# Kernel tuning notes

Hardware: AMD Instinct MI355X
Metric: run time of the kernel (lower is better)

Reference implementation:

```python
import jax, jax.numpy as jnp
import numpy as np

N_NODES = 100000
N_EDGES = 1600000
IN_DIM = 128
OUT_DIM = 64
HEADS = 4
NEG_SLOPE = 0.2  # PyG GATConv default
LN_EPS = 1e-5


def setup_inputs() -> dict:
    key = jax.random.key(0)
    ks = jax.random.split(key, 8)
    x = jax.random.normal(ks[0], (N_NODES, IN_DIM), dtype=jnp.float32)
    edge_index = jax.random.randint(ks[1], (2, N_EDGES), 0, N_NODES, dtype=jnp.int64)
    # GATConv params: lin weight, per-head attention vectors, output bias (concat=False)
    s = 1.0 / np.sqrt(IN_DIM)
    W = jax.random.uniform(ks[2], (IN_DIM, HEADS * OUT_DIM), jnp.float32, -s, s)
    att_src = jax.random.uniform(ks[3], (HEADS, OUT_DIM), jnp.float32, -s, s)
    att_dst = jax.random.uniform(ks[4], (HEADS, OUT_DIM), jnp.float32, -s, s)
    bias = jnp.zeros((OUT_DIM,), jnp.float32)
    gamma = jnp.ones((OUT_DIM,), jnp.float32)
    beta = jnp.zeros((OUT_DIM,), jnp.float32)
    return {"x": x, "edge_index": edge_index, "W": W, "att_src": att_src,
            "att_dst": att_dst, "bias": bias, "gamma": gamma, "beta": beta}


def reference(x, edge_index, W, att_src, att_dst, bias, gamma, beta):
    N = x.shape[0]
    H, C = att_src.shape
    # Linear projection, split heads: (N, H, C)
    xl = (x @ W).reshape(N, H, C)
    # Per-node attention logits: (N, H)
    a_src = jnp.einsum('nhc,hc->nh', xl, att_src)
    a_dst = jnp.einsum('nhc,hc->nh', xl, att_dst)
    # Add self-loops (PyG GATConv default add_self_loops=True)
    loops = jnp.arange(N, dtype=edge_index.dtype)
    src = jnp.concatenate([edge_index[0], loops])  # (E+N,)
    dst = jnp.concatenate([edge_index[1], loops])
    # Per-edge attention: gather, leaky_relu, segment softmax over destination
    alpha = jax.nn.leaky_relu(a_src[src] + a_dst[dst], NEG_SLOPE)  # (E+N, H)
    amax = jax.ops.segment_max(alpha, dst, num_segments=N)  # (N, H)
    e = jnp.exp(alpha - amax[dst])
    denom = jax.ops.segment_sum(e, dst, num_segments=N)  # (N, H)
    alpha = e / (denom[dst] + 1e-16)
    # Message passing: scatter-add alpha-weighted source features to dst
    msg = xl[src] * alpha[:, :, None]  # (E+N, H, C)
    out = jax.ops.segment_sum(msg, dst, num_segments=N)  # (N, H, C)
    out = out.mean(axis=1) + bias  # concat=False -> head average, (N, C)
    # LayerNorm
    mu = out.mean(axis=-1, keepdims=True)
    var = out.var(axis=-1, keepdims=True)
    return (out - mu) * jax.lax.rsqrt(var + LN_EPS) * gamma + beta
```

## Files before the change

### kernel.cpp

```cpp
#include <hip/hip_runtime.h>
#include <hip/hip_fp16.h>

#define IN_DIM   128
#define HC       256
#define OUT_DIM  64
#define HEADS    4
#define NEG_SLOPE 0.2f
#define LN_EPS   1e-5f
#define MAXBINS  512
#define NHIST    128
#define SCAT_TPE 16

typedef short bf16x8 __attribute__((ext_vector_type(8)));
typedef float f32x4  __attribute__((ext_vector_type(4)));

__device__ __forceinline__ float lrelu(float a){ return a > 0.f ? a : NEG_SLOPE * a; }

__device__ __forceinline__ unsigned short f2bf(float f){
  unsigned u = __float_as_uint(f);
  u = u + 0x7fffu + ((u >> 16) & 1u);
  return (unsigned short)(u >> 16);
}
__device__ __forceinline__ unsigned pk2(float a, float b){
  return (unsigned)f2bf(a) | ((unsigned)f2bf(b) << 16);
}
__device__ __forceinline__ __half2 u2h(unsigned u){ return *(__half2*)&u; }
__device__ __forceinline__ unsigned h2u(__half2 h){ return *(unsigned*)&h; }

__device__ __forceinline__ bool detect32(const int* ei){
  int ln = threadIdx.x & 63;
  unsigned probe = (ln < 32) ? (unsigned)ei[2*ln + 1] : 0u;
  return __ballot(probe != 0) != 0ull;
}

__global__ __launch_bounds__(256) void k_front(
    const float* __restrict__ W, unsigned short* __restrict__ Wt,
    const int* ei, int* __restrict__ partials, int E, int nbins)
{
  if (blockIdx.x < 128){
    int n = blockIdx.x*2 + (threadIdx.x >> 7);
    int k = threadIdx.x & 127;
    Wt[n*IN_DIM + k] = f2bf(W[k*HC + n]);
    return;
  }
  __shared__ int h[MAXBINS];
  bool i32 = detect32(ei);
  for (int i = threadIdx.x; i < nbins; i += 256) h[i] = 0;
  __syncthreads();
  int slot = blockIdx.x - 128;
  if (i32){
    const int* dstp = ei + E;
    for (int e = slot*256 + threadIdx.x; e < E; e += NHIST*256)
      atomicAdd(&h[dstp[e] >> 8], 1);
  } else {
    const long long* dstp = (const long long*)ei + E;
    for (int e = slot*256 + threadIdx.x; e < E; e += NHIST*256)
      atomicAdd(&h[(int)dstp[e] >> 8], 1);
  }
  __syncthreads();
  for (int i = threadIdx.x; i < nbins; i += 256)
    partials[slot*MAXBINS + i] = h[i];
}

__global__ __launch_bounds__(512) void k_binscan(const int* __restrict__ partials,
    int* binstart, int* bincur, int* rowstart, int nbins, int N, int E){
  __shared__ int sh[512];
  int tid = threadIdx.x;
  int v = 0;
  if (tid < nbins)
    for (int j = 0; j < NHIST; ++j) v += partials[j*MAXBINS + tid];
  sh[tid] = v; __syncthreads();
  #pragma unroll
  for (int off = 1; off < 512; off <<= 1){
    int t = (tid >= off) ? sh[tid-off] : 0;
    __syncthreads();
    sh[tid] += t;
    __syncthreads();
  }
  int ex = sh[tid] - v;
  if (tid < nbins){ binstart[tid] = ex; bincur[tid] = ex; }
  if (tid == 0){ binstart[nbins] = E; rowstart[N] = E; }
}

__device__ __forceinline__ void gemm_body(int bid, char* smem,
    const float* __restrict__ x, const unsigned short* __restrict__ Wt,
    const float* __restrict__ att_s, const float* __restrict__ att_d,
    __half* __restrict__ xl_t, float* __restrict__ a_src,
    float* __restrict__ a_dst, int N)
{
  unsigned short* sxl = (unsigned short*)(smem + 16384);
  int t = threadIdx.x;
  int nb = bid * 64;

  #pragma unroll
  for (int it = 0; it < 4; ++it){
    int idx = it*256 + t;
    int row = idx >> 4, seg = idx & 15;
    uint4 pk = make_uint4(0,0,0,0);
    if (nb + row < N){
      const float* xr = x + (size_t)(nb + row)*IN_DIM + seg*8;
      float4 f0 = *(const float4*)xr;
      float4 f1 = *(const float4*)(xr + 4);
      pk.x = pk2(f0.x, f0.y); pk.y = pk2(f0.z, f0.w);
      pk.z = pk2(f1.x, f1.y); pk.w = pk2(f1.z, f1.w);
    }
    int byte = (row*256 + seg*16) ^ ((row & 7) << 4);
    *(uint4*)(smem + byte) = pk;
  }
  __syncthreads();

  int w = t >> 6, l = t & 63;

  bf16x8 bfr[4][4];
  #pragma unroll
  for (int nt = 0; nt < 4; ++nt){
    int col = w*64 + nt*16 + (l & 15);
    #pragma unroll
    for (int ks = 0; ks < 4; ++ks)
      bfr[nt][ks] = *(const bf16x8*)(Wt + (size_t)col*IN_DIM + ks*32 + ((l >> 4) << 3));
  }
  float attS[4], attD[4];
  #pragma unroll
  for (int nt = 0; nt < 4; ++nt){
    attS[nt] = att_s[w*64 + nt*16 + (l & 15)];
    attD[nt] = att_d[w*64 + nt*16 + (l & 15)];
  }

  #pragma unroll
  for (int sub = 0; sub < 4; ++sub){
    bf16x8 afr[4];
    #pragma unroll
    for (int ks = 0; ks < 4; ++ks){
      int row = sub*16 + (l & 15);
      int byte = (row*256 + ks*64 + ((l >> 4) << 4)) ^ ((row & 7) << 4);
      afr[ks] = *(const bf16x8*)(smem + byte);
    }
    f32x4 acc[4] = {{0,0,0,0},{0,0,0,0},{0,0,0,0},{0,0,0,0}};
    #pragma unroll
    for (int nt = 0; nt < 4; ++nt)
      #pragma unroll
      for (int ks = 0; ks < 4; ++ks)
        acc[nt] = __builtin_amdgcn_mfma_f32_16x16x32_bf16(afr[ks], bfr[nt][ks], acc[nt], 0, 0, 0);

    #pragma unroll
    for (int r = 0; r < 4; ++r){
      float ps = 0.f, pd = 0.f;
      #pragma unroll
      for (int nt = 0; nt < 4; ++nt){
        ps = fmaf(acc[nt][r], attS[nt], ps);
        pd = fmaf(acc[nt][r], attD[nt], pd);
      }
      #pragma unroll
      for (int o = 8; o; o >>= 1){ ps += __shfl_xor(ps, o); pd += __shfl_xor(pd, o); }
      int node = nb + sub*16 + (l >> 4)*4 + r;
      if ((l & 15) == 0 && node < N){
        a_src[node*4 + w] = ps;
        a_dst[node*4 + w] = pd;
      }
    }

    #pragma unroll
    for (int nt = 0; nt < 4; ++nt){
      int ch = nt*16 + (l & 15);
      #pragma unroll
      for (int r = 0; r < 4; ++r){
        int row = sub*16 + (l >> 4)*4 + r;
        sxl[row*HC + ch*4 + w] = __half_as_ushort(__float2half(acc[nt][r]));
      }
    }
  }
  __syncthreads();
  const uint4* s4 = (const uint4*)sxl;
  uint4* g4 = (uint4*)(xl_t + (size_t)nb*HC);
  for (int c = t; c < 2048; c += 256){
    int row = c >> 5;
    if (nb + row < N) g4[c] = s4[c];
  }
}

__device__ __forceinline__ void scat_body(int bid, char* smem,
    const int* ei, int* bincur, unsigned* tmp, int E, int nbins)
{
  int* h    = (int*)smem;
  int* base = (int*)(smem + 2048);
  bool i32 = detect32(ei);
  int tile0 = bid * (256*SCAT_TPE);
  for (int i = threadIdx.x; i < nbins; i += 256) h[i] = 0;
  __syncthreads();
  unsigned pk[SCAT_TPE]; int rk[SCAT_TPE];
  #pragma unroll
  for (int k = 0; k < SCAT_TPE; ++k){
    int e = tile0 + k*256 + threadIdx.x;
    if (e < E){
      int s, d;
      if (i32){ s = ei[e]; d = ei[E + e]; }
      else {
        s = (int)((const long long*)ei)[e];
        d = (int)((const long long*)ei)[(size_t)E + e];
      }
      int b = d >> 8;
      pk[k] = (unsigned)s | ((unsigned)(d & 255) << 20);
      rk[k] = atomicAdd(&h[b], 1) | (b << 16);
    }
  }
  __syncthreads();
  for (int i = threadIdx.x; i < nbins; i += 256)
    base[i] = h[i] ? atomicAdd(&bincur[i], h[i]) : 0;
  __syncthreads();
  #pragma unroll
  for (int k = 0; k < SCAT_TPE; ++k){
    int e = tile0 + k*256 + threadIdx.x;
    if (e < E){
      int b = rk[k] >> 16, r = rk[k] & 0xFFFF;
      tmp[base[b] + r] = pk[k];
    }
  }
}

__global__ __launch_bounds__(256) void k_gemm_scat(
    const float* __restrict__ x, const unsigned short* __restrict__ Wt,
    const float* __restrict__ att_s, const float* __restrict__ att_d,
    __half* __restrict__ xl_t, float* __restrict__ a_src, float* __restrict__ a_dst,
    int N, const int* ei, int* bincur, unsigned* tmp, int E, int nbins,
    int gemmBlocks)
{
  __shared__ char smem[49152];
  int bid = (int)blockIdx.x;
  if (bid < gemmBlocks)
    gemm_body(bid, smem, x, Wt, att_s, att_d, xl_t, a_src, a_dst, N);
  else
    scat_body(bid - gemmBlocks, smem, ei, bincur, tmp, E, nbins);
}

__global__ __launch_bounds__(256) void k_binsort(const unsigned* __restrict__ tmp,
    const int* __restrict__ binstart, int* rowstart, int* csr, int N){
  __shared__ int c[256], c2[256], sc[256];
  int b = blockIdx.x, tid = threadIdx.x;
  int s0 = binstart[b], s1 = binstart[b+1];
  c[tid] = 0; c2[tid] = 0;
  __syncthreads();
  for (int e = s0 + tid; e < s1; e += 256)
    atomicAdd(&c[(tmp[e] >> 20) & 255], 1);
  __syncthreads();
  int v = c[tid]; sc[tid] = v;
  __syncthreads();
  #pragma unroll
  for (int off = 1; off < 256; off <<= 1){
    int t = (tid >= off) ? sc[tid-off] : 0;
    __syncthreads();
    sc[tid] += t;
    __syncthreads();
  }
  int ex = sc[tid] - v;
  int d = b*256 + tid;
  if (d < N) rowstart[d] = s0 + ex;
  sc[tid] = ex;
  __syncthreads();
  for (int e = s0 + tid; e < s1; e += 256){
    unsigned u = tmp[e];
    int dl = (u >> 20) & 255;
    int pos = s0 + sc[dl] + atomicAdd(&c2[dl], 1);
    csr[pos] = (int)(u & 0xFFFFFu);
  }
}

__global__ __launch_bounds__(256) void k_node(
    const int* __restrict__ rowstart, const int* __restrict__ csr,
    const float4* __restrict__ a_src4, const float4* __restrict__ a_dst4,
    const __half* __restrict__ xl_t,
    const float* __restrict__ bias, const float* __restrict__ gamma,
    const float* __restrict__ beta, float* __restrict__ out, int N)
{
  __shared__ uint2 wlds[4][4][16];
  __shared__ int   slds[4][4][16];
  int wv = threadIdx.x >> 6, ln = threadIdx.x & 63;
  int g = ln >> 4, i = ln & 15;
  int node = blockIdx.x*16 + wv*4 + g;
  bool alive = node < N;
  int nc = alive ? node : N-1;

  int start = rowstart[nc];
  int end   = alive ? rowstart[nc+1] : start;
  float4 ad  = a_dst4[nc];
  float4 asl = a_src4[nc];

  float es0 = __expf(lrelu(asl.x + ad.x));
  float es1 = __expf(lrelu(asl.y + ad.y));
  float es2 = __expf(lrelu(asl.z + ad.z));
  float es3 = __expf(lrelu(asl.w + ad.w));

  __half2 s01 = __floats2half2_rn(es0, es1);
  __half2 s23 = __floats2half2_rn(es2, es3);
  const uint4* ps = (const uint4*)((const char*)xl_t + ((size_t)nc*512 + (i << 5)));
  uint4 xa = ps[0], xb = ps[1];
  __half2 acc[8];
  acc[0] = __hmul2(s01, u2h(xa.x));
  acc[1] = __hmul2(s23, u2h(xa.y));
  acc[2] = __hmul2(s01, u2h(xa.z));
  acc[3] = __hmul2(s23, u2h(xa.w));
  acc[4] = __hmul2(s01, u2h(xb.x));
  acc[5] = __hmul2(s23, u2h(xb.y));
  acc[6] = __hmul2(s01, u2h(xb.z));
  acc[7] = __hmul2(s23, u2h(xb.w));
  float lp0 = 0.f, lp1 = 0.f, lp2 = 0.f, lp3 = 0.f;

  for (int t = start; ; t += 16){
    int rem = end - t;
    rem = rem < 0 ? 0 : (rem > 16 ? 16 : rem);
    int rmax = rem;
    rmax = max(rmax, __shfl_xor(rmax, 16));
    rmax = max(rmax, __shfl_xor(rmax, 32));
    if (rmax == 0) break;

    int sid = 0;
    float e0 = 0.f, e1 = 0.f, e2 = 0.f, e3 = 0.f;
    if (i < rem){
      sid = csr[t + i];
      float4 as4 = a_src4[sid];
      e0 = __expf(lrelu(as4.x + ad.x));
      e1 = __expf(lrelu(as4.y + ad.y));
      e2 = __expf(lrelu(as4.z + ad.z));
      e3 = __expf(lrelu(as4.w + ad.w));
      lp0 += e0; lp1 += e1; lp2 += e2; lp3 += e3;
    }
    wlds[wv][g][i] = make_uint2(h2u(__floats2half2_rn(e0, e1)),
                                h2u(__floats2half2_rn(e2, e3)));
    slds[wv][g][i] = sid;

    #pragma unroll 2
    for (int j = 0; j < rmax; ++j){
      if (j < rem){
        uint2 wpk = wlds[wv][g][j];
        int sj = slds[wv][g][j];
        __half2 w01 = u2h(wpk.x), w23 = u2h(wpk.y);
        const uint4* p = (const uint4*)((const char*)xl_t + ((size_t)sj*512 + (i << 5)));
        uint4 ya = p[0], yb = p[1];
        acc[0] = __hfma2(w01, u2h(ya.x), acc[0]);
        acc[1] = __hfma2(w23, u2h(ya.y), acc[1]);
        acc[2] = __hfma2(w01, u2h(ya.z), acc[2]);
        acc[3] = __hfma2(w23, u2h(ya.w), acc[3]);
        acc[4] = __hfma2(w01, u2h(yb.x), acc[4]);
        acc[5] = __hfma2(w23, u2h(yb.y), acc[5]);
        acc[6] = __hfma2(w01, u2h(yb.z), acc[6]);
        acc[7] = __hfma2(w23, u2h(yb.w), acc[7]);
      }
    }
  }

  __half2 lp01 = __floats2half2_rn(lp0, lp1);
  __half2 lp23 = __floats2half2_rn(lp2, lp3);
  #pragma unroll
  for (int o = 8; o; o >>= 1){
    lp01 = __hadd2(lp01, u2h(__shfl_xor(h2u(lp01), o)));
    lp23 = __hadd2(lp23, u2h(__shfl_xor(h2u(lp23), o)));
  }
  float r0 = __builtin_amdgcn_rcpf(__low2float(lp01) + es0);
  float r1 = __builtin_amdgcn_rcpf(__high2float(lp01) + es1);
  float r2 = __builtin_amdgcn_rcpf(__low2float(lp23) + es2);
  float r3 = __builtin_amdgcn_rcpf(__high2float(lp23) + es3);

  float4 b4 = *(const float4*)(bias + 4*i);
  float o0 = 0.25f*(__low2float(acc[0])*r0 + __high2float(acc[0])*r1 +
                    __low2float(acc[1])*r2 + __high2float(acc[1])*r3) + b4.x;
  float o1 = 0.25f*(__low2float(acc[2])*r0 + __high2float(acc[2])*r1 +
                    __low2float(acc[3])*r2 + __high2float(acc[3])*r3) + b4.y;
  float o2 = 0.25f*(__low2float(acc[4])*r0 + __high2float(acc[4])*r1 +
                    __low2float(acc[5])*r2 + __high2float(acc[5])*r3) + b4.z;
  float o3 = 0.25f*(__low2float(acc[6])*r0 + __high2float(acc[6])*r1 +
                    __low2float(acc[7])*r2 + __high2float(acc[7])*r3) + b4.w;

  float s  = o0 + o1 + o2 + o3;
  float sq = o0*o0 + o1*o1 + o2*o2 + o3*o3;
  #pragma unroll
  for (int o = 8; o; o >>= 1){
    s  += __shfl_xor(s, o);
    sq += __shfl_xor(sq, o);
  }
  float mu = s * (1.f/OUT_DIM);
  float var = sq * (1.f/OUT_DIM) - mu*mu;
  float rs = rsqrtf(var + LN_EPS);
  float4 g4v = *(const float4*)(gamma + 4*i);
  float4 be4 = *(const float4*)(beta + 4*i);
  if (alive){
    float4 ov;
    ov.x = (o0 - mu)*rs*g4v.x + be4.x;
    ov.y = (o1 - mu)*rs*g4v.y + be4.y;
    ov.z = (o2 - mu)*rs*g4v.z + be4.z;
    ov.w = (o3 - mu)*rs*g4v.w + be4.w;
    *(float4*)(out + (size_t)node*OUT_DIM + 4*i) = ov;
  }
}

extern "C" void kernel_launch(void* const* d_in, const int* in_sizes, int n_in,
                              void* d_out, int out_size, void* d_ws, size_t ws_size,
                              hipStream_t stream)
{
  const float* x     = (const float*)d_in[0];
  const int*   ei    = (const int*)d_in[1];
  const float* W     = (const float*)d_in[2];
  const float* att_s = (const float*)d_in[3];
  const float* att_d = (const float*)d_in[4];
  const float* bias  = (const float*)d_in[5];
  const float* gamma = (const float*)d_in[6];
  const float* beta  = (const float*)d_in[7];
  float* out = (float*)d_out;

  int N = in_sizes[0] / IN_DIM;
  int E = in_sizes[1] / 2;
  int nbins = (N + 255) >> 8;

  char* ws = (char*)d_ws;
  __half* xl_t = (__half*)ws;                   ws += (size_t)N*HC*sizeof(__half);
  float* a_src = (float*)ws;                    ws += (size_t)N*HEADS*sizeof(float);
  float* a_dst = (float*)ws;                    ws += (size_t)N*HEADS*sizeof(float);
  int* rowstart = (int*)ws;                     ws += ((size_t)N+1)*sizeof(int);
  int* csr      = (int*)ws;                     ws += (size_t)E*sizeof(int);
  unsigned* tmp = (unsigned*)ws;                ws += (size_t)E*sizeof(unsigned);
  int* partials = (int*)ws;                     ws += (size_t)NHIST*MAXBINS*sizeof(int);
  int* binstart = (int*)ws;                     ws += (MAXBINS+1)*sizeof(int);
  int* bincur   = (int*)ws;                     ws += MAXBINS*sizeof(int);
  unsigned short* Wt = (unsigned short*)ws;     ws += (size_t)HC*IN_DIM*sizeof(unsigned short);

  int gemmBlocks = (N + 63)/64;
  int scatBlocks = (E + 256*SCAT_TPE - 1)/(256*SCAT_TPE);

  k_front   <<<128 + NHIST, 256, 0, stream>>>(W, Wt, ei, partials, E, nbins);
  k_binscan <<<1, 512, 0, stream>>>(partials, binstart, bincur, rowstart, nbins, N, E);
  k_gemm_scat<<<gemmBlocks + scatBlocks, 256, 0, stream>>>(
      x, Wt, att_s, att_d, xl_t, a_src, a_dst, N, ei, bincur, tmp, E, nbins,
      gemmBlocks);
  k_binsort <<<nbins, 256, 0, stream>>>(tmp, binstart, rowstart, csr, N);
  k_node    <<<(N + 15)/16, 256, 0, stream>>>(rowstart, csr,
              (const float4*)a_src, (const float4*)a_dst, xl_t,
              bias, gamma, beta, out, N);
}
```

Baseline: 221.8 us.

## Fuse per-bin CSR sort into node aggregation kernel with 64-node bins

Shrinks destination bins from 256 to 64 nodes and merges the bin-local counting sort into the aggregation kernel, building each bin's CSR segment in shared memory instead of writing and rereading a global CSR and rowstart. Bin histograms are now combined with global atomics after a memset rather than through a partials array, and the scan is widened to 1024 threads for up to 2048 bins. The GEMM epilogue now streams each 16-row subtile out through a smaller LDS buffer, halving the kernel's static shared memory. In exchange, each node block does more serial work over fewer, larger blocks (one per 64 nodes, 4 nodes per 16-lane group sequentially), which may reduce parallelism and latency hiding in the gather phase.

```diff
diff --git a/kernel.cpp b/kernel.cpp
--- a/kernel.cpp
+++ b/kernel.cpp
@@ -7,8 +7,11 @@
 #define HEADS    4
 #define NEG_SLOPE 0.2f
 #define LN_EPS   1e-5f
-#define MAXBINS  512
-#define NHIST    128
+#define DBITS    6
+#define DPB      64
+#define MAXBINS  2048
+#define CAP      2048
+#define NHIST    256
 #define SCAT_TPE 16
 
 typedef short bf16x8 __attribute__((ext_vector_type(8)));
@@ -35,7 +38,7 @@
 
 __global__ __launch_bounds__(256) void k_front(
     const float* __restrict__ W, unsigned short* __restrict__ Wt,
-    const int* ei, int* __restrict__ partials, int E, int nbins)
+    const int* ei, int* __restrict__ bincnt, int E, int nbins)
 {
   if (blockIdx.x < 128){
     int n = blockIdx.x*2 + (threadIdx.x >> 7);
@@ -51,35 +54,38 @@
   if (i32){
     const int* dstp = ei + E;
     for (int e = slot*256 + threadIdx.x; e < E; e += NHIST*256)
-      atomicAdd(&h[dstp[e] >> 8], 1);
+      atomicAdd(&h[dstp[e] >> DBITS], 1);
   } else {
     const long long* dstp = (const long long*)ei + E;
     for (int e = slot*256 + threadIdx.x; e < E; e += NHIST*256)
-      atomicAdd(&h[(int)dstp[e] >> 8], 1);
+      atomicAdd(&h[((int)dstp[e]) >> DBITS], 1);
   }
   __syncthreads();
   for (int i = threadIdx.x; i < nbins; i += 256)
-    partials[slot*MAXBINS + i] = h[i];
-}
-
-__global__ __launch_bounds__(512) void k_binscan(const int* __restrict__ partials,
-    int* binstart, int* bincur, int* rowstart, int nbins, int N, int E){
-  __shared__ int sh[512];
-  int tid = threadIdx.x;
-  int v = 0;
-  if (tid < nbins)
-    for (int j = 0; j < NHIST; ++j) v += partials[j*MAXBINS + tid];
-  sh[tid] = v; __syncthreads();
-  #pragma unroll
-  for (int off = 1; off < 512; off <<= 1){
-    int t = (tid >= off) ? sh[tid-off] : 0;
-    __syncthreads();
-    sh[tid] += t;
-    __syncthreads();
-  }
-  int ex = sh[tid] - v;
-  if (tid < nbins){ binstart[tid] = ex; bincur[tid] = ex; }
-  if (tid == 0){ binstart[nbins] = E; rowstart[N] = E; }
+    if (h[i]) atomicAdd(&bincnt[i], h[i]);
+}
+
+__global__ __launch_bounds__(1024) void k_binscan(const int* __restrict__ bincnt,
+    int* binstart, int* bincur, int nbins, int E)
+{
+  __shared__ int sh[1024];
+  int t = threadIdx.x;
+  int i0 = 2*t, i1 = 2*t + 1;
+  int a = (i0 < nbins) ? bincnt[i0] : 0;
+  int b = (i1 < nbins) ? bincnt[i1] : 0;
+  int s = a + b;
+  sh[t] = s; __syncthreads();
+  #pragma unroll
+  for (int off = 1; off < 1024; off <<= 1){
+    int v = (t >= off) ? sh[t-off] : 0;
+    __syncthreads();
+    sh[t] += v;
+    __syncthreads();
+  }
+  int ex = sh[t] - s;
+  if (i0 < nbins){ binstart[i0] = ex;     bincur[i0] = ex; }
+  if (i1 < nbins){ binstart[i1] = ex + a; bincur[i1] = ex + a; }
+  if (t == 0) binstart[nbins] = E;
 }
 
 __device__ __forceinline__ void gemm_body(int bid, char* smem,
@@ -164,17 +170,19 @@
       int ch = nt*16 + (l & 15);
       #pragma unroll
       for (int r = 0; r < 4; ++r){
-        int row = sub*16 + (l >> 4)*4 + r;
+        int row = (l >> 4)*4 + r;
         sxl[row*HC + ch*4 + w] = __half_as_ushort(__float2half(acc[nt][r]));
       }
     }
-  }
-  __syncthreads();
-  const uint4* s4 = (const uint4*)sxl;
-  uint4* g4 = (uint4*)(xl_t + (size_t)nb*HC);
-  for (int c = t; c < 2048; c += 256){
-    int row = c >> 5;
-    if (nb + row < N) g4[c] = s4[c];
+    __syncthreads();
+    const uint4* s4 = (const uint4*)sxl;
+    uint4* g4 = (uint4*)(xl_t + (size_t)(nb + sub*16)*HC);
+    #pragma unroll
+    for (int c = t; c < 512; c += 256){
+      int row = c >> 5;
+      if (nb + sub*16 + row < N) g4[c] = s4[c];
+    }
+    __syncthreads();
   }
 }
 
@@ -182,7 +190,7 @@
     const int* ei, int* bincur, unsigned* tmp, int E, int nbins)
 {
   int* h    = (int*)smem;
-  int* base = (int*)(smem + 2048);
+  int* base = (int*)(smem + MAXBINS*4);
   bool i32 = detect32(ei);
   int tile0 = bid * (256*SCAT_TPE);
   for (int i = threadIdx.x; i < nbins; i += 256) h[i] = 0;
@@ -198,8 +206,8 @@
         s = (int)((const long long*)ei)[e];
         d = (int)((const long long*)ei)[(size_t)E + e];
       }
-      int b = d >> 8;
-      pk[k] = (unsigned)s | ((unsigned)(d & 255) << 20);
+      int b = d >> DBITS;
+      pk[k] = (unsigned)s | ((unsigned)(d & (DPB-1)) << 20);
       rk[k] = atomicAdd(&h[b], 1) | (b << 16);
     }
   }
@@ -224,7 +232,7 @@
     int N, const int* ei, int* bincur, unsigned* tmp, int E, int nbins,
     int gemmBlocks)
 {
-  __shared__ char smem[49152];
+  __shared__ char smem[24576];
   int bid = (int)blockIdx.x;
   if (bid < gemmBlocks)
     gemm_body(bid, smem, x, Wt, att_s, att_d, xl_t, a_src, a_dst, N);
@@ -232,106 +240,95 @@
     scat_body(bid - gemmBlocks, smem, ei, bincur, tmp, E, nbins);
 }
 
-__global__ __launch_bounds__(256) void k_binsort(const unsigned* __restrict__ tmp,
-    const int* __restrict__ binstart, int* rowstart, int* csr, int N){
-  __shared__ int c[256], c2[256], sc[256];
-  int b = blockIdx.x, tid = threadIdx.x;
-  int s0 = binstart[b], s1 = binstart[b+1];
-  c[tid] = 0; c2[tid] = 0;
-  __syncthreads();
-  for (int e = s0 + tid; e < s1; e += 256)
-    atomicAdd(&c[(tmp[e] >> 20) & 255], 1);
-  __syncthreads();
-  int v = c[tid]; sc[tid] = v;
-  __syncthreads();
-  #pragma unroll
-  for (int off = 1; off < 256; off <<= 1){
-    int t = (tid >= off) ? sc[tid-off] : 0;
-    __syncthreads();
-    sc[tid] += t;
-    __syncthreads();
-  }
-  int ex = sc[tid] - v;
-  int d = b*256 + tid;
-  if (d < N) rowstart[d] = s0 + ex;
-  sc[tid] = ex;
-  __syncthreads();
-  for (int e = s0 + tid; e < s1; e += 256){
-    unsigned u = tmp[e];
-    int dl = (u >> 20) & 255;
-    int pos = s0 + sc[dl] + atomicAdd(&c2[dl], 1);
-    csr[pos] = (int)(u & 0xFFFFFu);
-  }
-}
-
 __global__ __launch_bounds__(256) void k_node(
-    const int* __restrict__ rowstart, const int* __restrict__ csr,
+    const int* __restrict__ binstart, const unsigned* __restrict__ tmp,
+    int* __restrict__ csr,
     const float4* __restrict__ a_src4, const float4* __restrict__ a_dst4,
     const __half* __restrict__ xl_t,
     const float* __restrict__ bias, const float* __restrict__ gamma,
     const float* __restrict__ beta, float* __restrict__ out, int N)
 {
-  __shared__ uint2 wlds[4][4][16];
-  __shared__ int   slds[4][4][16];
-  int wv = threadIdx.x >> 6, ln = threadIdx.x & 63;
-  int g = ln >> 4, i = ln & 15;
-  int node = blockIdx.x*16 + wv*4 + g;
-  bool alive = node < N;
-  int nc = alive ? node : N-1;
-
-  int start = rowstart[nc];
-  int end   = alive ? rowstart[nc+1] : start;
-  float4 ad  = a_dst4[nc];
-  float4 asl = a_src4[nc];
-
-  float es0 = __expf(lrelu(asl.x + ad.x));
-  float es1 = __expf(lrelu(asl.y + ad.y));
-  float es2 = __expf(lrelu(asl.z + ad.z));
-  float es3 = __expf(lrelu(asl.w + ad.w));
-
-  __half2 s01 = __floats2half2_rn(es0, es1);
-  __half2 s23 = __floats2half2_rn(es2, es3);
-  const uint4* ps = (const uint4*)((const char*)xl_t + ((size_t)nc*512 + (i << 5)));
-  uint4 xa = ps[0], xb = ps[1];
-  __half2 acc[8];
-  acc[0] = __hmul2(s01, u2h(xa.x));
-  acc[1] = __hmul2(s23, u2h(xa.y));
-  acc[2] = __hmul2(s01, u2h(xa.z));
-  acc[3] = __hmul2(s23, u2h(xa.w));
-  acc[4] = __hmul2(s01, u2h(xb.x));
-  acc[5] = __hmul2(s23, u2h(xb.y));
-  acc[6] = __hmul2(s01, u2h(xb.z));
-  acc[7] = __hmul2(s23, u2h(xb.w));
-  float lp0 = 0.f, lp1 = 0.f, lp2 = 0.f, lp3 = 0.f;
-
-  for (int t = start; ; t += 16){
-    int rem = end - t;
-    rem = rem < 0 ? 0 : (rem > 16 ? 16 : rem);
-    int rmax = rem;
-    rmax = max(rmax, __shfl_xor(rmax, 16));
-    rmax = max(rmax, __shfl_xor(rmax, 32));
-    if (rmax == 0) break;
-
-    int sid = 0;
-    float e0 = 0.f, e1 = 0.f, e2 = 0.f, e3 = 0.f;
-    if (i < rem){
-      sid = csr[t + i];
-      float4 as4 = a_src4[sid];
-      e0 = __expf(lrelu(as4.x + ad.x));
-      e1 = __expf(lrelu(as4.y + ad.y));
-      e2 = __expf(lrelu(as4.z + ad.z));
-      e3 = __expf(lrelu(as4.w + ad.w));
-      lp0 += e0; lp1 += e1; lp2 += e2; lp3 += e3;
-    }
-    wlds[wv][g][i] = make_uint2(h2u(__floats2half2_rn(e0, e1)),
-                                h2u(__floats2half2_rn(e2, e3)));
-    slds[wv][g][i] = sid;
-
-    #pragma unroll 2
-    for (int j = 0; j < rmax; ++j){
-      if (j < rem){
-        uint2 wpk = wlds[wv][g][j];
-        int sj = slds[wv][g][j];
+  __shared__ int cnt[DPB], sc[DPB], cur[DPB];
+  __shared__ int lcsr[CAP];
+  __shared__ uint2 wlds[16][16];
+  int b = blockIdx.x, tid = threadIdx.x;
+  int s0 = binstart[b], s1 = binstart[b+1];
+  int seg = s1 - s0;
+
+  if (tid < DPB) cnt[tid] = 0;
+  __syncthreads();
+  for (int e = s0 + tid; e < s1; e += 256)
+    atomicAdd(&cnt[(tmp[e] >> 20) & (DPB-1)], 1);
+  __syncthreads();
+  if (tid < DPB) sc[tid] = cnt[tid];
+  __syncthreads();
+  #pragma unroll
+  for (int off = 1; off < DPB; off <<= 1){
+    int v = (tid < DPB && tid >= off) ? sc[tid-off] : 0;
+    __syncthreads();
+    if (tid < DPB) sc[tid] += v;
+    __syncthreads();
+  }
+  if (tid < DPB){ int ex = sc[tid] - cnt[tid]; sc[tid] = ex; cur[tid] = ex; }
+  __syncthreads();
+
+  int* ebuf = (seg <= CAP) ? lcsr : (csr + s0);
+  for (int e = s0 + tid; e < s1; e += 256){
+    unsigned u = tmp[e];
+    int dl = (u >> 20) & (DPB-1);
+    int r = atomicAdd(&cur[dl], 1);
+    ebuf[r] = (int)(u & 0xFFFFFu);
+  }
+  __syncthreads();
+
+  int gg = tid >> 4, i = tid & 15;
+  for (int n = 0; n < 4; ++n){
+    int dl = gg*4 + n;
+    int node = b*DPB + dl;
+    if (node >= N) continue;
+    int lstart = sc[dl], lend = lstart + cnt[dl];
+
+    float4 ad  = a_dst4[node];
+    float4 asl = a_src4[node];
+    float es0 = __expf(lrelu(asl.x + ad.x));
+    float es1 = __expf(lrelu(asl.y + ad.y));
+    float es2 = __expf(lrelu(asl.z + ad.z));
+    float es3 = __expf(lrelu(asl.w + ad.w));
+
+    __half2 s01 = __floats2half2_rn(es0, es1);
+    __half2 s23 = __floats2half2_rn(es2, es3);
+    const uint4* ps = (const uint4*)((const char*)xl_t + ((size_t)node*512 + (i << 5)));
+    uint4 xa = ps[0], xb = ps[1];
+    __half2 acc[8];
+    acc[0] = __hmul2(s01, u2h(xa.x));
+    acc[1] = __hmul2(s23, u2h(xa.y));
+    acc[2] = __hmul2(s01, u2h(xa.z));
+    acc[3] = __hmul2(s23, u2h(xa.w));
+    acc[4] = __hmul2(s01, u2h(xb.x));
+    acc[5] = __hmul2(s23, u2h(xb.y));
+    acc[6] = __hmul2(s01, u2h(xb.z));
+    acc[7] = __hmul2(s23, u2h(xb.w));
+    float lp0 = 0.f, lp1 = 0.f, lp2 = 0.f, lp3 = 0.f;
+
+    for (int t2 = lstart; t2 < lend; t2 += 16){
+      int rem = lend - t2; if (rem > 16) rem = 16;
+      float e0 = 0.f, e1 = 0.f, e2 = 0.f, e3 = 0.f;
+      if (i < rem){
+        int sid = ebuf[t2 + i];
+        float4 as4 = a_src4[sid];
+        e0 = __expf(lrelu(as4.x + ad.x));
+        e1 = __expf(lrelu(as4.y + ad.y));
+        e2 = __expf(lrelu(as4.z + ad.z));
+        e3 = __expf(lrelu(as4.w + ad.w));
+        lp0 += e0; lp1 += e1; lp2 += e2; lp3 += e3;
+      }
+      wlds[gg][i] = make_uint2(h2u(__floats2half2_rn(e0, e1)),
+                               h2u(__floats2half2_rn(e2, e3)));
+
+      #pragma unroll 2
+      for (int j = 0; j < rem; ++j){
+        uint2 wpk = wlds[gg][j];
+        int sj = ebuf[t2 + j];
         __half2 w01 = u2h(wpk.x), w23 = u2h(wpk.y);
         const uint4* p = (const uint4*)((const char*)xl_t + ((size_t)sj*512 + (i << 5)));
         uint4 ya = p[0], yb = p[1];
@@ -345,43 +342,41 @@
         acc[7] = __hfma2(w23, u2h(yb.w), acc[7]);
       }
     }
-  }
-
-  __half2 lp01 = __floats2half2_rn(lp0, lp1);
-  __half2 lp23 = __floats2half2_rn(lp2, lp3);
-  #pragma unroll
-  for (int o = 8; o; o >>= 1){
-    lp01 = __hadd2(lp01, u2h(__shfl_xor(h2u(lp01), o)));
-    lp23 = __hadd2(lp23, u2h(__shfl_xor(h2u(lp23), o)));
-  }
-  float r0 = __builtin_amdgcn_rcpf(__low2float(lp01) + es0);
-  float r1 = __builtin_amdgcn_rcpf(__high2float(lp01) + es1);
-  float r2 = __builtin_amdgcn_rcpf(__low2float(lp23) + es2);
-  float r3 = __builtin_amdgcn_rcpf(__high2float(lp23) + es3);
-
-  float4 b4 = *(const float4*)(bias + 4*i);
-  float o0 = 0.25f*(__low2float(acc[0])*r0 + __high2float(acc[0])*r1 +
-                    __low2float(acc[1])*r2 + __high2float(acc[1])*r3) + b4.x;
-  float o1 = 0.25f*(__low2float(acc[2])*r0 + __high2float(acc[2])*r1 +
-                    __low2float(acc[3])*r2 + __high2float(acc[3])*r3) + b4.y;
-  float o2 = 0.25f*(__low2float(acc[4])*r0 + __high2float(acc[4])*r1 +
-                    __low2float(acc[5])*r2 + __high2float(acc[5])*r3) + b4.z;
-  float o3 = 0.25f*(__low2float(acc[6])*r0 + __high2float(acc[6])*r1 +
-                    __low2float(acc[7])*r2 + __high2float(acc[7])*r3) + b4.w;
-
-  float s  = o0 + o1 + o2 + o3;
-  float sq = o0*o0 + o1*o1 + o2*o2 + o3*o3;
-  #pragma unroll
-  for (int o = 8; o; o >>= 1){
-    s  += __shfl_xor(s, o);
-    sq += __shfl_xor(sq, o);
-  }
-  float mu = s * (1.f/OUT_DIM);
-  float var = sq * (1.f/OUT_DIM) - mu*mu;
-  float rs = rsqrtf(var + LN_EPS);
-  float4 g4v = *(const float4*)(gamma + 4*i);
-  float4 be4 = *(const float4*)(beta + 4*i);
-  if (alive){
+
+    __half2 lp01 = __floats2half2_rn(lp0, lp1);
+    __half2 lp23 = __floats2half2_rn(lp2, lp3);
+    #pragma unroll
+    for (int o = 8; o; o >>= 1){
+      lp01 = __hadd2(lp01, u2h(__shfl_xor(h2u(lp01), o)));
+      lp23 = __hadd2(lp23, u2h(__shfl_xor(h2u(lp23), o)));
+    }
+    float r0 = __builtin_amdgcn_rcpf(__low2float(lp01) + es0);
+    float r1 = __builtin_amdgcn_rcpf(__high2float(lp01) + es1);
+    float r2 = __builtin_amdgcn_rcpf(__low2float(lp23) + es2);
+    float r3 = __builtin_amdgcn_rcpf(__high2float(lp23) + es3);
+
+    float4 b4 = *(const float4*)(bias + 4*i);
+    float o0 = 0.25f*(__low2float(acc[0])*r0 + __high2float(acc[0])*r1 +
+                      __low2float(acc[1])*r2 + __high2float(acc[1])*r3) + b4.x;
+    float o1 = 0.25f*(__low2float(acc[2])*r0 + __high2float(acc[2])*r1 +
+                      __low2float(acc[3])*r2 + __high2float(acc[3])*r3) + b4.y;
+    float o2 = 0.25f*(__low2float(acc[4])*r0 + __high2float(acc[4])*r1 +
+                      __low2float(acc[5])*r2 + __high2float(acc[5])*r3) + b4.z;
+    float o3 = 0.25f*(__low2float(acc[6])*r0 + __high2float(acc[6])*r1 +
+                      __low2float(acc[7])*r2 + __high2float(acc[7])*r3) + b4.w;
+
+    float s  = o0 + o1 + o2 + o3;
+    float sq = o0*o0 + o1*o1 + o2*o2 + o3*o3;
+    #pragma unroll
+    for (int o = 8; o; o >>= 1){
+      s  += __shfl_xor(s, o);
+      sq += __shfl_xor(sq, o);
+    }
+    float mu = s * (1.f/OUT_DIM);
+    float var = sq * (1.f/OUT_DIM) - mu*mu;
+    float rs = rsqrtf(var + LN_EPS);
+    float4 g4v = *(const float4*)(gamma + 4*i);
+    float4 be4 = *(const float4*)(beta + 4*i);
     float4 ov;
     ov.x = (o0 - mu)*rs*g4v.x + be4.x;
     ov.y = (o1 - mu)*rs*g4v.y + be4.y;
@@ -407,16 +402,15 @@
 
   int N = in_sizes[0] / IN_DIM;
   int E = in_sizes[1] / 2;
-  int nbins = (N + 255) >> 8;
+  int nbins = (N + DPB - 1) >> DBITS;
 
   char* ws = (char*)d_ws;
   __half* xl_t = (__half*)ws;                   ws += (size_t)N*HC*sizeof(__half);
   float* a_src = (float*)ws;                    ws += (size_t)N*HEADS*sizeof(float);
   float* a_dst = (float*)ws;                    ws += (size_t)N*HEADS*sizeof(float);
-  int* rowstart = (int*)ws;                     ws += ((size_t)N+1)*sizeof(int);
   int* csr      = (int*)ws;                     ws += (size_t)E*sizeof(int);
   unsigned* tmp = (unsigned*)ws;                ws += (size_t)E*sizeof(unsigned);
-  int* partials = (int*)ws;                     ws += (size_t)NHIST*MAXBINS*sizeof(int);
+  int* bincnt   = (int*)ws;                     ws += MAXBINS*sizeof(int);
   int* binstart = (int*)ws;                     ws += (MAXBINS+1)*sizeof(int);
   int* bincur   = (int*)ws;                     ws += MAXBINS*sizeof(int);
   unsigned short* Wt = (unsigned short*)ws;     ws += (size_t)HC*IN_DIM*sizeof(unsigned short);
@@ -424,13 +418,13 @@
   int gemmBlocks = (N + 63)/64;
   int scatBlocks = (E + 256*SCAT_TPE - 1)/(256*SCAT_TPE);
 
-  k_front   <<<128 + NHIST, 256, 0, stream>>>(W, Wt, ei, partials, E, nbins);
-  k_binscan <<<1, 512, 0, stream>>>(partials, binstart, bincur, rowstart, nbins, N, E);
+  hipMemsetAsync(bincnt, 0, (size_t)nbins*sizeof(int), stream);
+  k_front   <<<128 + NHIST, 256, 0, stream>>>(W, Wt, ei, bincnt, E, nbins);
+  k_binscan <<<1, 1024, 0, stream>>>(bincnt, binstart, bincur, nbins, E);
   k_gemm_scat<<<gemmBlocks + scatBlocks, 256, 0, stream>>>(
       x, Wt, att_s, att_d, xl_t, a_src, a_dst, N, ei, bincur, tmp, E, nbins,
       gemmBlocks);
-  k_binsort <<<nbins, 256, 0, stream>>>(tmp, binstart, rowstart, csr, N);
-  k_node    <<<(N + 15)/16, 256, 0, stream>>>(rowstart, csr,
+  k_node    <<<nbins, 256, 0, stream>>>(binstart, tmp, csr,
               (const float4*)a_src, (const float4*)a_dst, xl_t,
               bias, gamma, beta, out, N);
 }
```

Measured after the change: 221.3 us. No clear change (-0.2%).
